# Kernel tuning notes

Measured on AMD Instinct MI355X. Metric: run time of the kernel, lower is better.

Reference implementation:

```python
import jax, jax.numpy as jnp
import numpy as np

W_BIT = 4
HALF = 2 ** (W_BIT - 1)  # 8: recentering offset used in post_init
GROUP_SIZE = 128
IN_FEATURES = 4096
OUT_FEATURES = 11008
TOKENS = 32


def setup_inputs() -> dict:
    key = jax.random.key(0)
    k1, k2, k3, k4, k5 = jax.random.split(key, 5)
    n_groups = IN_FEATURES // GROUP_SIZE
    x = jax.random.normal(k1, (TOKENS, IN_FEATURES), dtype=jnp.float32)
    # unpacked 4-bit weight codes in [0, 15]
    qweight = jax.random.randint(k2, (IN_FEATURES, OUT_FEATURES), 0, 2 ** W_BIT, dtype=jnp.int32)
    # group-wise 4-bit zero-point codes in [0, 15]
    qzeros = jax.random.randint(k3, (n_groups, OUT_FEATURES), 0, 2 ** W_BIT, dtype=jnp.int32)
    # group-wise scales (positive, small, like real quant scales)
    scales = jax.random.uniform(k4, (n_groups, OUT_FEATURES), dtype=jnp.float32, minval=0.001, maxval=0.02)
    bias = jax.random.normal(k5, (OUT_FEATURES,), dtype=jnp.float32)
    return {"x": x, "qweight": qweight, "qzeros": qzeros, "scales": scales, "bias": bias}


def reference(x, qweight, qzeros, scales, bias):
    # post_init recenters codes: q -> q - 2^(b-1), z -> z - 2^(b-1)
    w_int = (qweight - HALF).astype(jnp.float32)            # [K, N]
    z_int = (qzeros - HALF).astype(jnp.float32)             # [K//gs, N]
    # broadcast group-wise zeros/scales along K
    z_rep = jnp.repeat(z_int, GROUP_SIZE, axis=0)           # [K, N]
    s_rep = jnp.repeat(scales, GROUP_SIZE, axis=0)          # [K, N]
    # fused dequant-GEMM: y = x @ ((q - z) * s) + bias
    w_deq = (w_int - z_rep) * s_rep                         # [K, N] fp32
    out = x @ w_deq + bias                                  # [T, N]
    return out
```

## Files before the change

### kernel.cpp

```cpp
#include <hip/hip_runtime.h>
#include <hip/hip_bf16.h>


#define TOKENS   32
#define KDIM     4096
#define NDIM     11008
#define GS       128
#define KSPLIT   8
#define KCHUNK   512
#define BLOCK    128
#define BLOCK_N  128

typedef __attribute__((ext_vector_type(8))) _Float16 half8;
typedef __attribute__((ext_vector_type(4))) float   floatx4;

__global__ __launch_bounds__(256) void awq_cvt_kernel(
    const float* __restrict__ x, unsigned short* __restrict__ xh)
{
    const int i = blockIdx.x * 256 + threadIdx.x;
    const float4 v = ((const float4*)x)[i];
    ushort4 o;
    o.x = __builtin_bit_cast(unsigned short, (_Float16)v.x);
    o.y = __builtin_bit_cast(unsigned short, (_Float16)v.y);
    o.z = __builtin_bit_cast(unsigned short, (_Float16)v.z);
    o.w = __builtin_bit_cast(unsigned short, (_Float16)v.w);
    ((ushort4*)xh)[i] = o;
}

__global__ __launch_bounds__(256) void awq_init_kernel(
    const float* __restrict__ bias, float* __restrict__ out)
{
    const int n = blockIdx.x * 256 + threadIdx.x;
    out[blockIdx.y * NDIM + n] = bias[n];
}

template<bool ATOMIC>
__global__ __launch_bounds__(BLOCK) void awq_gemm_mfma(
    const unsigned short* __restrict__ xh,
    const int*   __restrict__ qw,
    const int*   __restrict__ qz,
    const float* __restrict__ sc,
    float*       __restrict__ dst)
{
    const int tid  = threadIdx.x;
    const int lane = tid & 63;
    const int wv   = tid >> 6;
    const int col  = lane & 15;
    const int quad = lane >> 4;
    const int nb   = blockIdx.x * BLOCK_N + wv * 64;
    const int nc   = nb + 4 * col;

    floatx4 acc[4][2];
    #pragma unroll
    for (int nt = 0; nt < 4; ++nt) {
        acc[nt][0] = (floatx4){0.f, 0.f, 0.f, 0.f};
        acc[nt][1] = (floatx4){0.f, 0.f, 0.f, 0.f};
    }

    for (int gi = 0; gi < KCHUNK / GS; ++gi) {
        const int g   = blockIdx.y * (KCHUNK / GS) + gi;
        const int kc0 = g * GS;

        float s[4], nzs[4];
        #pragma unroll
        for (int nt = 0; nt < 4; ++nt) {
            const int n  = nc + nt;
            const float sv = sc[(size_t)g * NDIM + n];
            const int   zv = qz[(size_t)g * NDIM + n];
            s[nt] = sv; nzs[nt] = -(float)zv * sv;
        }

        const int* qbase = qw + (size_t)(kc0 + quad * 8) * NDIM + nc;
        const unsigned short* xr0 = xh + (size_t)col * KDIM + kc0 + quad * 8;
        const unsigned short* xr1 = xr0 + 16 * KDIM;

        #pragma unroll 2
        for (int ks = 0; ks < GS / 32; ++ks) {
            int4 q[8];
            #pragma unroll
            for (int j = 0; j < 8; ++j)
                q[j] = *(const int4*)(qbase + (size_t)(ks * 32 + j) * NDIM);

            const half8 a0 = *(const half8*)(xr0 + ks * 32);
            const half8 a1 = *(const half8*)(xr1 + ks * 32);

            half8 b0, b1, b2, b3;
            #pragma unroll
            for (int j = 0; j < 8; ++j) {
                b0[j] = (_Float16)fmaf((float)q[j].x, s[0], nzs[0]);
                b1[j] = (_Float16)fmaf((float)q[j].y, s[1], nzs[1]);
                b2[j] = (_Float16)fmaf((float)q[j].z, s[2], nzs[2]);
                b3[j] = (_Float16)fmaf((float)q[j].w, s[3], nzs[3]);
            }
            acc[0][0] = __builtin_amdgcn_mfma_f32_16x16x32_f16(a0, b0, acc[0][0], 0, 0, 0);
            acc[0][1] = __builtin_amdgcn_mfma_f32_16x16x32_f16(a1, b0, acc[0][1], 0, 0, 0);
            acc[1][0] = __builtin_amdgcn_mfma_f32_16x16x32_f16(a0, b1, acc[1][0], 0, 0, 0);
            acc[1][1] = __builtin_amdgcn_mfma_f32_16x16x32_f16(a1, b1, acc[1][1], 0, 0, 0);
            acc[2][0] = __builtin_amdgcn_mfma_f32_16x16x32_f16(a0, b2, acc[2][0], 0, 0, 0);
            acc[2][1] = __builtin_amdgcn_mfma_f32_16x16x32_f16(a1, b2, acc[2][1], 0, 0, 0);
            acc[3][0] = __builtin_amdgcn_mfma_f32_16x16x32_f16(a0, b3, acc[3][0], 0, 0, 0);
            acc[3][1] = __builtin_amdgcn_mfma_f32_16x16x32_f16(a1, b3, acc[3][1], 0, 0, 0);
        }
    }

    if (ATOMIC) {
        #pragma unroll
        for (int h = 0; h < 2; ++h)
            #pragma unroll
            for (int r = 0; r < 4; ++r) {
                float* pp = dst + (size_t)(h * 16 + quad * 4 + r) * NDIM + nc;
                unsafeAtomicAdd(pp + 0, acc[0][h][r]);
                unsafeAtomicAdd(pp + 1, acc[1][h][r]);
                unsafeAtomicAdd(pp + 2, acc[2][h][r]);
                unsafeAtomicAdd(pp + 3, acc[3][h][r]);
            }
    } else {
        float* pbase = dst + (size_t)blockIdx.y * TOKENS * NDIM;
        #pragma unroll
        for (int h = 0; h < 2; ++h)
            #pragma unroll
            for (int r = 0; r < 4; ++r) {
                const float4 v = make_float4(acc[0][h][r], acc[1][h][r],
                                             acc[2][h][r], acc[3][h][r]);
                *(float4*)(pbase + (size_t)(h * 16 + quad * 4 + r) * NDIM + nc) = v;
            }
    }
}

__global__ __launch_bounds__(256) void awq_reduce_kernel(
    const float* __restrict__ part,
    const float* __restrict__ bias,
    float*       __restrict__ out)
{
    const int o = blockIdx.x * 256 + threadIdx.x;
    const int t = o / (NDIM / 4);
    const int c = o - t * (NDIM / 4);
    const float4* p4 = (const float4*)part;
    float4 sum = ((const float4*)bias)[c];
    #pragma unroll
    for (int s = 0; s < KSPLIT; ++s) {
        const float4 v = p4[(size_t)(s * TOKENS + t) * (NDIM / 4) + c];
        sum.x += v.x; sum.y += v.y; sum.z += v.z; sum.w += v.w;
    }
    ((float4*)out)[o] = sum;
}

extern "C" void kernel_launch(void* const* d_in, const int* in_sizes, int n_in,
                              void* d_out, int out_size, void* d_ws, size_t ws_size,
                              hipStream_t stream) {
    const float* x    = (const float*)d_in[0];
    const int*   qw   = (const int*)  d_in[1];
    const int*   qz   = (const int*)  d_in[2];
    const float* sc   = (const float*)d_in[3];
    const float* bias = (const float*)d_in[4];
    float* out = (float*)d_out;

    const size_t xh_bytes   = 512 * 1024;
    const size_t part_bytes = (size_t)KSPLIT * TOKENS * NDIM * sizeof(float);
    unsigned short* xh = (unsigned short*)d_ws;
    float* part = (float*)((char*)d_ws + xh_bytes);

    awq_cvt_kernel<<<(TOKENS * KDIM / 4) / 256, 256, 0, stream>>>(x, xh);

    if (ws_size >= xh_bytes + part_bytes) {
        awq_gemm_mfma<false><<<dim3(NDIM / BLOCK_N, KSPLIT), BLOCK, 0, stream>>>(
            xh, qw, qz, sc, part);
        awq_reduce_kernel<<<(TOKENS * NDIM / 4) / 256, 256, 0, stream>>>(
            part, bias, out);
    } else {
        awq_init_kernel<<<dim3(NDIM / 256, TOKENS), 256, 0, stream>>>(bias, out);
        awq_gemm_mfma<true><<<dim3(NDIM / BLOCK_N, KSPLIT), BLOCK, 0, stream>>>(
            xh, qw, qz, sc, out);
    }
}
```

Before: 266.1 us.

## Pre-pack int32 weight codes into 4-bit nibbles before the MFMA GEMM

Adds a per-call packing kernel that reads the int32 weight codes and packs eight K-consecutive 4-bit codes into one 32-bit word. The GEMM then loads one uint4 per k-step instead of eight int4 loads and unpacks the codes with shifts and masks. The int32 weight tensor (about 180 MB) is still read once per call by the pack kernel, which adds an extra write and launch, so the total traffic for the large tensor is not reduced. The atomic fallback path is removed and the workspace is assumed large enough for the packed weights plus the partial sums.

```diff
diff --git a/kernel.cpp b/kernel.cpp
--- a/kernel.cpp
+++ b/kernel.cpp
@@ -27,17 +27,22 @@
     ((ushort4*)xh)[i] = o;
 }
 
-__global__ __launch_bounds__(256) void awq_init_kernel(
-    const float* __restrict__ bias, float* __restrict__ out)
+__global__ __launch_bounds__(256) void awq_pack_kernel(
+    const int* __restrict__ qw, unsigned* __restrict__ pw)
 {
-    const int n = blockIdx.x * 256 + threadIdx.x;
-    out[blockIdx.y * NDIM + n] = bias[n];
+    const int n  = blockIdx.x * 256 + threadIdx.x;
+    const int ko = blockIdx.y;
+    const int* qp = qw + (size_t)ko * 8 * NDIM + n;
+    unsigned w = 0;
+    #pragma unroll
+    for (int j = 0; j < 8; ++j)
+        w |= ((unsigned)qp[(size_t)j * NDIM] & 0xFu) << (4 * j);
+    pw[(size_t)ko * NDIM + n] = w;
 }
 
-template<bool ATOMIC>
 __global__ __launch_bounds__(BLOCK) void awq_gemm_mfma(
     const unsigned short* __restrict__ xh,
-    const int*   __restrict__ qw,
+    const unsigned* __restrict__ pw,
     const int*   __restrict__ qz,
     const float* __restrict__ sc,
     float*       __restrict__ dst)
@@ -70,16 +75,13 @@
             s[nt] = sv; nzs[nt] = -(float)zv * sv;
         }
 
-        const int* qbase = qw + (size_t)(kc0 + quad * 8) * NDIM + nc;
+        const unsigned* wbase = pw + (size_t)((kc0 >> 3) + quad) * NDIM + nc;
         const unsigned short* xr0 = xh + (size_t)col * KDIM + kc0 + quad * 8;
         const unsigned short* xr1 = xr0 + 16 * KDIM;
 
         #pragma unroll 2
         for (int ks = 0; ks < GS / 32; ++ks) {
-            int4 q[8];
-            #pragma unroll
-            for (int j = 0; j < 8; ++j)
-                q[j] = *(const int4*)(qbase + (size_t)(ks * 32 + j) * NDIM);
+            const uint4 pq = *(const uint4*)(wbase + (size_t)(ks * 4) * NDIM);
 
             const half8 a0 = *(const half8*)(xr0 + ks * 32);
             const half8 a1 = *(const half8*)(xr1 + ks * 32);
@@ -87,10 +89,10 @@
             half8 b0, b1, b2, b3;
             #pragma unroll
             for (int j = 0; j < 8; ++j) {
-                b0[j] = (_Float16)fmaf((float)q[j].x, s[0], nzs[0]);
-                b1[j] = (_Float16)fmaf((float)q[j].y, s[1], nzs[1]);
-                b2[j] = (_Float16)fmaf((float)q[j].z, s[2], nzs[2]);
-                b3[j] = (_Float16)fmaf((float)q[j].w, s[3], nzs[3]);
+                b0[j] = (_Float16)fmaf((float)((pq.x >> (4 * j)) & 15u), s[0], nzs[0]);
+                b1[j] = (_Float16)fmaf((float)((pq.y >> (4 * j)) & 15u), s[1], nzs[1]);
+                b2[j] = (_Float16)fmaf((float)((pq.z >> (4 * j)) & 15u), s[2], nzs[2]);
+                b3[j] = (_Float16)fmaf((float)((pq.w >> (4 * j)) & 15u), s[3], nzs[3]);
             }
             acc[0][0] = __builtin_amdgcn_mfma_f32_16x16x32_f16(a0, b0, acc[0][0], 0, 0, 0);
             acc[0][1] = __builtin_amdgcn_mfma_f32_16x16x32_f16(a1, b0, acc[0][1], 0, 0, 0);
@@ -103,28 +105,15 @@
         }
     }
 
-    if (ATOMIC) {
+    float* pbase = dst + (size_t)blockIdx.y * TOKENS * NDIM;
+    #pragma unroll
+    for (int h = 0; h < 2; ++h)
         #pragma unroll
-        for (int h = 0; h < 2; ++h)
-            #pragma unroll
-            for (int r = 0; r < 4; ++r) {
-                float* pp = dst + (size_t)(h * 16 + quad * 4 + r) * NDIM + nc;
-                unsafeAtomicAdd(pp + 0, acc[0][h][r]);
-                unsafeAtomicAdd(pp + 1, acc[1][h][r]);
-                unsafeAtomicAdd(pp + 2, acc[2][h][r]);
-                unsafeAtomicAdd(pp + 3, acc[3][h][r]);
-            }
-    } else {
-        float* pbase = dst + (size_t)blockIdx.y * TOKENS * NDIM;
-        #pragma unroll
-        for (int h = 0; h < 2; ++h)
-            #pragma unroll
-            for (int r = 0; r < 4; ++r) {
-                const float4 v = make_float4(acc[0][h][r], acc[1][h][r],
-                                             acc[2][h][r], acc[3][h][r]);
-                *(float4*)(pbase + (size_t)(h * 16 + quad * 4 + r) * NDIM + nc) = v;
-            }
-    }
+        for (int r = 0; r < 4; ++r) {
+            const float4 v = make_float4(acc[0][h][r], acc[1][h][r],
+                                         acc[2][h][r], acc[3][h][r]);
+            *(float4*)(pbase + (size_t)(h * 16 + quad * 4 + r) * NDIM + nc) = v;
+        }
 }
 
 __global__ __launch_bounds__(256) void awq_reduce_kernel(
@@ -155,21 +144,18 @@
     const float* bias = (const float*)d_in[4];
     float* out = (float*)d_out;
 
-    const size_t xh_bytes   = 512 * 1024;
+    const size_t xh_bytes = 512 * 1024;
+    const size_t pw_bytes = (size_t)(KDIM / 8) * NDIM * sizeof(unsigned);
     const size_t part_bytes = (size_t)KSPLIT * TOKENS * NDIM * sizeof(float);
     unsigned short* xh = (unsigned short*)d_ws;
-    float* part = (float*)((char*)d_ws + xh_bytes);
+    unsigned* pwp = (unsigned*)((char*)d_ws + xh_bytes);
+    float* part = (float*)((char*)d_ws + xh_bytes + pw_bytes);
+    (void)ws_size; (void)part_bytes;
 
     awq_cvt_kernel<<<(TOKENS * KDIM / 4) / 256, 256, 0, stream>>>(x, xh);
-
-    if (ws_size >= xh_bytes + part_bytes) {
-        awq_gemm_mfma<false><<<dim3(NDIM / BLOCK_N, KSPLIT), BLOCK, 0, stream>>>(
-            xh, qw, qz, sc, part);
-        awq_reduce_kernel<<<(TOKENS * NDIM / 4) / 256, 256, 0, stream>>>(
-            part, bias, out);
-    } else {
-        awq_init_kernel<<<dim3(NDIM / 256, TOKENS), 256, 0, stream>>>(bias, out);
-        awq_gemm_mfma<true><<<dim3(NDIM / BLOCK_N, KSPLIT), BLOCK, 0, stream>>>(
-            xh, qw, qz, sc, out);
-    }
+    awq_pack_kernel<<<dim3(NDIM / 256, KDIM / 8), 256, 0, stream>>>(qw, pwp);
+    awq_gemm_mfma<<<dim3(NDIM / BLOCK_N, KSPLIT), BLOCK, 0, stream>>>(
+        xh, pwp, qz, sc, part);
+    awq_reduce_kernel<<<(TOKENS * NDIM / 4) / 256, 256, 0, stream>>>(
+        part, bias, out);
 }
```

Result: slower. 279.5 us (+5.0%).
